# Kernel tuning notes

Measured on AMD Instinct MI355X. Metric: run time of the kernel, lower is better.

## Reference

```python
import jax, jax.numpy as jnp
import numpy as np

N_CLASS = 50257
EMB = 512
HID = 512
B = 64
T = 256


def setup_inputs() -> dict:
    key = jax.random.key(0)
    ks = jax.random.split(key, 12)
    K = 1.0 / np.sqrt(HID)
    u = lambda k, shape: jax.random.uniform(k, shape, jnp.float32) * K
    return {
        "X": jax.random.randint(ks[0], (B, T), 0, N_CLASS, jnp.int32),
        "emb": jax.random.normal(ks[1], (N_CLASS, EMB), jnp.float32),
        "w_ih0": u(ks[2], (4 * HID, EMB)),
        "w_hh0": u(ks[3], (4 * HID, HID)),
        "b_ih0": u(ks[4], (4 * HID,)),
        "b_hh0": u(ks[5], (4 * HID,)),
        "w_ih1": u(ks[6], (4 * HID, HID)),
        "w_hh1": u(ks[7], (4 * HID, HID)),
        "b_ih1": u(ks[8], (4 * HID,)),
        "b_hh1": u(ks[9], (4 * HID,)),
        "W": jax.random.normal(ks[10], (N_CLASS, HID), jnp.float32) / np.sqrt(HID),
        "b": jnp.ones((N_CLASS,), jnp.float32),
    }


def _lstm_layer(x, w_ih, w_hh, b_ih, b_hh):
    # x: [B, T, in] -> outputs: [B, T, H]; gate order i, f, g, o (as in source slicing)
    H = w_hh.shape[1]
    # precompute input contribution + both biases for all timesteps (one big GEMM)
    xg = jnp.einsum("bti,gi->btg", x, w_ih) + b_ih + b_hh  # [B, T, 4H]

    def step(carry, xg_t):
        h, c = carry
        g = xg_t + h @ w_hh.T  # [B, 4H]
        i_t = jax.nn.sigmoid(g[:, :H])
        f_t = jax.nn.sigmoid(g[:, H:2 * H])
        g_t = jnp.tanh(g[:, 2 * H:3 * H])
        o_t = jax.nn.sigmoid(g[:, 3 * H:])
        c = f_t * c + i_t * g_t
        h = o_t * jnp.tanh(c)
        return (h, c), h

    bsz = x.shape[0]
    init = (jnp.zeros((bsz, H), x.dtype), jnp.zeros((bsz, H), x.dtype))
    _, ys = jax.lax.scan(step, init, jnp.swapaxes(xg, 0, 1))  # [T, B, H]
    return jnp.swapaxes(ys, 0, 1)


def reference(X, emb, w_ih0, w_hh0, b_ih0, b_hh0, w_ih1, w_hh1, b_ih1, b_hh1, W, b):
    x = emb[X]  # [B, T, EMB] embedding lookup
    h0 = _lstm_layer(x, w_ih0, w_hh0, b_ih0, b_hh0)   # layer 0
    h1 = _lstm_layer(h0, w_ih1, w_hh1, b_ih1, b_hh1)  # layer 1 (input = layer0 output)
    last = h1[:, -1, :]  # last timestep, [B, H]
    return last @ W.T + b  # [B, N_CLASS]
```

## Files before the change

kernel.cpp:

```cpp
#include <hip/hip_runtime.h>
#include <cstdint>
#include <cstddef>

#define HH 512
#define BB 64
#define TT 256
#define GG 2048
#define NCLS 50257
#define NWG 128

typedef __attribute__((ext_vector_type(4))) float f32x4;
typedef __attribute__((ext_vector_type(8))) short bf16x8;
typedef __attribute__((ext_vector_type(4))) unsigned int u32x4;
typedef __attribute__((ext_vector_type(8))) unsigned int u32x8;

__device__ __forceinline__ unsigned short bf16_rn(float x){
    unsigned u = __float_as_uint(x);
    unsigned r = u + 0x7fffu + ((u >> 16) & 1u);
    return (unsigned short)(r >> 16);
}
__device__ __forceinline__ void split2(float x, unsigned short& hi, unsigned short& lo){
    unsigned short h = bf16_rn(x);
    float hf = __uint_as_float(((unsigned)h) << 16);
    lo = bf16_rn(x - hf);
    hi = h;
}
__device__ __forceinline__ bf16x8 mk8(unsigned a, unsigned b, unsigned c, unsigned d){
    u32x4 t; t[0]=a; t[1]=b; t[2]=c; t[3]=d;
    return __builtin_bit_cast(bf16x8, t);
}

__global__ __launch_bounds__(256) void split_bf16_k(
    const float* __restrict__ in, unsigned short* __restrict__ hi,
    unsigned short* __restrict__ lo, int n)
{
    int i = blockIdx.x * 256 + threadIdx.x;
    if (i < n){ unsigned short h, l; split2(in[i], h, l); hi[i] = h; lo[i] = l; }
}

__global__ __launch_bounds__(256,1) void lstm_scan_mfma(
    const float* __restrict__ xg,
    const unsigned short* __restrict__ Whi,
    const unsigned short* __restrict__ Wlo,
    unsigned* __restrict__ hpk,
    float* __restrict__ hseq,
    int* __restrict__ bar,
    int mode)
{
    __shared__ float gs[BB][17];
    const int tid  = threadIdx.x;
    const int lane = tid & 63, wv = tid >> 6;
    const int wg   = blockIdx.x;
    const int j0   = wg * 4;
    const int c16  = lane & 15, kg = lane >> 4;

    bf16x8 wbh[16], wbl[16];
    {
        const int grow = (c16 >> 2) * HH + j0 + (c16 & 3);
        const unsigned short* ph = Whi + (size_t)grow * HH + kg * 8;
        const unsigned short* pl = Wlo + (size_t)grow * HH + kg * 8;
        #pragma unroll
        for (int kt = 0; kt < 16; kt++){
            wbh[kt] = *(const bf16x8*)(ph + kt * 32);
            wbl[kt] = *(const bf16x8*)(pl + kt * 32);
        }
    }

    const int arow = wv * 16 + c16;
    const int xcol = (c16 >> 2) * HH + j0 + (c16 & 3);
    const int b0   = wv * 16 + kg * 4;
    const int ab   = tid >> 2, ad = tid & 3;

    float c_st = 0.f;

    f32x4 cur;
    {
        const float* xp = xg + xcol;
        cur[0] = xp[(size_t)(b0 + 0) * GG];
        cur[1] = xp[(size_t)(b0 + 1) * GG];
        cur[2] = xp[(size_t)(b0 + 2) * GG];
        cur[3] = xp[(size_t)(b0 + 3) * GG];
    }

    for (int t = 0; t < TT; t++){
        const unsigned* hin  = hpk + (size_t)(t & 1) * BB * HH;
        unsigned*       hout = hpk + (size_t)((t + 1) & 1) * BB * HH;

        f32x4 acc = cur;
        const unsigned* pa = hin + (size_t)arow * HH + kg * 8;
        #pragma unroll
        for (int kt = 0; kt < 16; kt++){
            u32x8 w = *(const u32x8*)(pa + kt * 32);
            unsigned h01 = __builtin_amdgcn_perm(w[1], w[0], 0x05040100u);
            unsigned h23 = __builtin_amdgcn_perm(w[3], w[2], 0x05040100u);
            unsigned h45 = __builtin_amdgcn_perm(w[5], w[4], 0x05040100u);
            unsigned h67 = __builtin_amdgcn_perm(w[7], w[6], 0x05040100u);
            unsigned l01 = __builtin_amdgcn_perm(w[1], w[0], 0x07060302u);
            unsigned l23 = __builtin_amdgcn_perm(w[3], w[2], 0x07060302u);
            unsigned l45 = __builtin_amdgcn_perm(w[5], w[4], 0x07060302u);
            unsigned l67 = __builtin_amdgcn_perm(w[7], w[6], 0x07060302u);
            bf16x8 a_h = mk8(h01, h23, h45, h67);
            bf16x8 a_l = mk8(l01, l23, l45, l67);
            acc = __builtin_amdgcn_mfma_f32_16x16x32_bf16(a_h, wbh[kt], acc, 0, 0, 0);
            acc = __builtin_amdgcn_mfma_f32_16x16x32_bf16(a_h, wbl[kt], acc, 0, 0, 0);
            acc = __builtin_amdgcn_mfma_f32_16x16x32_bf16(a_l, wbh[kt], acc, 0, 0, 0);
        }
        gs[b0 + 0][c16] = acc[0];
        gs[b0 + 1][c16] = acc[1];
        gs[b0 + 2][c16] = acc[2];
        gs[b0 + 3][c16] = acc[3];
        __syncthreads();
        {
            float gi = gs[ab][ad], gf = gs[ab][4 + ad], gg = gs[ab][8 + ad], go = gs[ab][12 + ad];
            gi = 1.f / (1.f + expf(-gi));
            gf = 1.f / (1.f + expf(-gf));
            gg = tanhf(gg);
            go = 1.f / (1.f + expf(-go));
            c_st = gf * c_st + gi * gg;
            float h = go * tanhf(c_st);
            unsigned short hb, lb; split2(h, hb, lb);
            unsigned pk = (((unsigned)lb) << 16) | (unsigned)hb;
            __hip_atomic_store(&hout[(size_t)ab * HH + j0 + ad], pk,
                               __ATOMIC_RELAXED, __HIP_MEMORY_SCOPE_AGENT);
            if (mode) hseq[(size_t)ab * TT * HH + (size_t)t * HH + j0 + ad] = h;
            else      hseq[(size_t)ab * HH + j0 + ad] = h;
        }
        __syncthreads();
        if (tid == 0){
            const int g = wg & 7;
            int old = __hip_atomic_fetch_add(bar + 32 + g * 32, 1,
                        __ATOMIC_RELAXED, __HIP_MEMORY_SCOPE_AGENT);
            if (old == (NWG / 8) * (t + 1) - 1){
                int r = __hip_atomic_fetch_add(bar + 288, 1,
                            __ATOMIC_RELAXED, __HIP_MEMORY_SCOPE_AGENT);
                if (r == 8 * (t + 1) - 1){
                    __hip_atomic_store(bar, t + 1,
                        __ATOMIC_RELAXED, __HIP_MEMORY_SCOPE_AGENT);
                }
            }
        }
        {
            const int tp = (t + 1 < TT) ? t + 1 : t;
            const float* xp = xg + (size_t)tp * BB * GG + xcol;
            cur[0] = xp[(size_t)(b0 + 0) * GG];
            cur[1] = xp[(size_t)(b0 + 1) * GG];
            cur[2] = xp[(size_t)(b0 + 2) * GG];
            cur[3] = xp[(size_t)(b0 + 3) * GG];
        }
        if (tid == 0){
            while (__hip_atomic_load(bar, __ATOMIC_RELAXED, __HIP_MEMORY_SCOPE_AGENT) < t + 1)
                __builtin_amdgcn_s_sleep(2);
            __builtin_amdgcn_fence(__ATOMIC_ACQUIRE, "agent");
        }
        __syncthreads();
    }
}

__global__ __launch_bounds__(256,2) void gemm_xg(
    const float* __restrict__ A, const int* __restrict__ gather,
    const float* __restrict__ Bw, const float* __restrict__ bias1,
    const float* __restrict__ bias2, float* __restrict__ out, int K)
{
    __shared__ float As[32][132];
    __shared__ float Bs[32][132];
    const int tid = threadIdx.x;
    const int row0 = blockIdx.y * 128, col0 = blockIdx.x * 128;
    const int tx = tid & 15, ty = tid >> 4;
    float acc[8][8];
    #pragma unroll
    for (int i=0;i<8;i++)
        #pragma unroll
        for (int j=0;j<8;j++) acc[i][j]=0.f;

    for (int k0=0;k0<K;k0+=32){
        #pragma unroll
        for (int i=0;i<4;i++){
            int f = tid + i*256;
            int r = f>>3, kq = f&7;
            const int grow = row0 + r;
            const float* src = gather ? (A + (size_t)gather[grow]*K)
                                      : (A + (size_t)grow*K);
            float4 v = *(const float4*)(src + k0 + kq*4);
            As[kq*4+0][r]=v.x; As[kq*4+1][r]=v.y; As[kq*4+2][r]=v.z; As[kq*4+3][r]=v.w;
        }
        #pragma unroll
        for (int i=0;i<4;i++){
            int f = tid + i*256;
            int r = f>>3, kq = f&7;
            const float* src = Bw + (size_t)(col0 + r)*K;
            float4 v = *(const float4*)(src + k0 + kq*4);
            Bs[kq*4+0][r]=v.x; Bs[kq*4+1][r]=v.y; Bs[kq*4+2][r]=v.z; Bs[kq*4+3][r]=v.w;
        }
        __syncthreads();
        #pragma unroll
        for (int kk=0;kk<32;kk++){
            float4 a03 = *(float4*)&As[kk][ty*8];
            float4 a47 = *(float4*)&As[kk][ty*8+4];
            float4 b03 = *(float4*)&Bs[kk][tx*8];
            float4 b47 = *(float4*)&Bs[kk][tx*8+4];
            float a[8] = {a03.x,a03.y,a03.z,a03.w,a47.x,a47.y,a47.z,a47.w};
            float b[8] = {b03.x,b03.y,b03.z,b03.w,b47.x,b47.y,b47.z,b47.w};
            #pragma unroll
            for (int i=0;i<8;i++)
                #pragma unroll
                for (int j=0;j<8;j++) acc[i][j] += a[i]*b[j];
        }
        __syncthreads();
    }
    #pragma unroll
    for (int i=0;i<8;i++){
        int r = row0 + ty*8 + i;
        int b = r >> 8, t = r & 255;
        float* orow = out + (size_t)(t*BB + b)*GG + col0 + tx*8;
        #pragma unroll
        for (int j=0;j<8;j++){
            int col = col0 + tx*8 + j;
            orow[j] = acc[i][j] + bias1[col] + bias2[col];
        }
    }
}

__global__ __launch_bounds__(256) void gemm_logits(
    const float* __restrict__ hlast, const float* __restrict__ W,
    const float* __restrict__ bias, float* __restrict__ out)
{
    __shared__ float As[32][68];
    __shared__ float Bs[32][68];
    const int tid = threadIdx.x;
    const int col0 = blockIdx.x * 64;
    const int tx = tid & 15, ty = tid >> 4;
    float acc[4][4];
    #pragma unroll
    for (int i=0;i<4;i++)
        #pragma unroll
        for (int j=0;j<4;j++) acc[i][j]=0.f;

    for (int k0=0;k0<HH;k0+=32){
        #pragma unroll
        for (int i=0;i<2;i++){
            int f = tid + i*256;
            int r = f>>3, kq = f&7;
            float4 v = *(const float4*)(hlast + (size_t)r*HH + k0 + kq*4);
            As[kq*4+0][r]=v.x; As[kq*4+1][r]=v.y; As[kq*4+2][r]=v.z; As[kq*4+3][r]=v.w;
        }
        #pragma unroll
        for (int i=0;i<2;i++){
            int f = tid + i*256;
            int r = f>>3, kq = f&7;
            int vrow = col0 + r;
            float4 v = make_float4(0.f,0.f,0.f,0.f);
            if (vrow < NCLS) v = *(const float4*)(W + (size_t)vrow*HH + k0 + kq*4);
            Bs[kq*4+0][r]=v.x; Bs[kq*4+1][r]=v.y; Bs[kq*4+2][r]=v.z; Bs[kq*4+3][r]=v.w;
        }
        __syncthreads();
        #pragma unroll
        for (int kk=0;kk<32;kk++){
            float4 a4 = *(float4*)&As[kk][ty*4];
            float4 b4 = *(float4*)&Bs[kk][tx*4];
            float a[4] = {a4.x,a4.y,a4.z,a4.w};
            float b[4] = {b4.x,b4.y,b4.z,b4.w};
            #pragma unroll
            for (int i=0;i<4;i++)
                #pragma unroll
                for (int j=0;j<4;j++) acc[i][j] += a[i]*b[j];
        }
        __syncthreads();
    }
    #pragma unroll
    for (int i=0;i<4;i++){
        int b = ty*4 + i;
        #pragma unroll
        for (int j=0;j<4;j++){
            int v = col0 + tx*4 + j;
            if (v < NCLS) out[(size_t)b*NCLS + v] = acc[i][j] + bias[v];
        }
    }
}

extern "C" void kernel_launch(void* const* d_in, const int* in_sizes, int n_in,
                              void* d_out, int out_size, void* d_ws, size_t ws_size,
                              hipStream_t stream)
{
    const int*   X     = (const int*)  d_in[0];
    const float* emb   = (const float*)d_in[1];
    const float* w_ih0 = (const float*)d_in[2];
    const float* w_hh0 = (const float*)d_in[3];
    const float* b_ih0 = (const float*)d_in[4];
    const float* b_hh0 = (const float*)d_in[5];
    const float* w_ih1 = (const float*)d_in[6];
    const float* w_hh1 = (const float*)d_in[7];
    const float* b_ih1 = (const float*)d_in[8];
    const float* b_hh1 = (const float*)d_in[9];
    const float* Wout  = (const float*)d_in[10];
    const float* bout  = (const float*)d_in[11];
    float* out = (float*)d_out;

    float* ws    = (float*)d_ws;
    float* xg    = ws;
    float* h0seq = ws + 33554432;
    float* hlast = ws + 41943040;
    unsigned short* Whi0 = (unsigned short*)(ws + 41975808);
    unsigned short* Wlo0 = (unsigned short*)(ws + 42500096);
    unsigned short* Whi1 = (unsigned short*)(ws + 43024384);
    unsigned short* Wlo1 = (unsigned short*)(ws + 43548672);
    unsigned*       hpk  = (unsigned*)(ws + 44072960);
    int*            bar  = (int*)(ws + 44138496);

    dim3 gemmGrid(16, 128);

    split_bf16_k<<<4096, 256, 0, stream>>>(w_hh0, Whi0, Wlo0, GG*HH);
    split_bf16_k<<<4096, 256, 0, stream>>>(w_hh1, Whi1, Wlo1, GG*HH);

    gemm_xg<<<gemmGrid, 256, 0, stream>>>(emb, X, w_ih0, b_ih0, b_hh0, xg, HH);
    hipMemsetAsync(hpk, 0, (size_t)2*BB*HH*sizeof(unsigned), stream);
    hipMemsetAsync(bar, 0, 4096, stream);
    {
        const float* a0 = xg; const unsigned short *a1 = Whi0, *a2 = Wlo0;
        unsigned* a3 = hpk; float* a4 = h0seq; int* a5 = bar; int a6 = 1;
        void* args[] = {&a0,&a1,&a2,&a3,&a4,&a5,&a6};
        hipLaunchCooperativeKernel((void*)lstm_scan_mfma, dim3(NWG), dim3(256), args, 0, stream);
    }
    gemm_xg<<<gemmGrid, 256, 0, stream>>>(h0seq, nullptr, w_ih1, b_ih1, b_hh1, xg, HH);
    hipMemsetAsync(hpk, 0, (size_t)2*BB*HH*sizeof(unsigned), stream);
    hipMemsetAsync(bar, 0, 4096, stream);
    {
        const float* a0 = xg; const unsigned short *a1 = Whi1, *a2 = Wlo1;
        unsigned* a3 = hpk; float* a4 = hlast; int* a5 = bar; int a6 = 0;
        void* args[] = {&a0,&a1,&a2,&a3,&a4,&a5,&a6};
        hipLaunchCooperativeKernel((void*)lstm_scan_mfma, dim3(NWG), dim3(256), args, 0, stream);
    }
    gemm_logits<<<786, 256, 0, stream>>>(hlast, Wout, bout, out);
}
```

Measured before the change: 4.944 ms.

## Use split-bf16 MFMA for input-projection GEMMs and stage recurrent weights in LDS

Replaces the scalar fp32 tiled input-projection GEMM with an MFMA kernel that uses a three-product hi/lo bf16 split, which keeps roughly fp32 accuracy. Layer-0 output is now stored as packed hi/lo bf16 so the layer-1 GEMM reads it without converting. The recurrent kernel moves its weight fragments from registers into LDS and splits accumulation across two accumulators so consecutive MFMAs do not depend on each other. Workspace buffers for the split weights are reused sequentially, which adds extra split launches and LDS reads on every timestep.

```diff
diff --git a/kernel.cpp b/kernel.cpp
--- a/kernel.cpp
+++ b/kernel.cpp
@@ -9,6 +9,9 @@
 #define NCLS 50257
 #define NWG 128
 
+#define PERM_HI 0x05040100u
+#define PERM_LO 0x07060302u
+
 typedef __attribute__((ext_vector_type(4))) float f32x4;
 typedef __attribute__((ext_vector_type(8))) short bf16x8;
 typedef __attribute__((ext_vector_type(4))) unsigned int u32x4;
@@ -38,15 +41,132 @@
     if (i < n){ unsigned short h, l; split2(in[i], h, l); hi[i] = h; lo[i] = l; }
 }
 
+__global__ __launch_bounds__(256,2) void gemm_xg_mfma(
+    const float* __restrict__ Af32, const unsigned* __restrict__ Apk,
+    const int* __restrict__ gather,
+    const unsigned short* __restrict__ Bhi, const unsigned short* __restrict__ Blo,
+    const float* __restrict__ bias1, const float* __restrict__ bias2,
+    float* __restrict__ out)
+{
+    __shared__ unsigned short Ah[128][40], Al[128][40], Bh[128][40], Bl[128][40];
+    const int tid  = threadIdx.x;
+    const int lane = tid & 63, wid = tid >> 6;
+    const int c16  = lane & 15, kg = lane >> 4;
+    const int row0 = blockIdx.y * 128, col0 = blockIdx.x * 128;
+    const int wm = (wid >> 1) * 64, wn = (wid & 1) * 64;
+    const int sr = tid & 127;
+    const bool isA = tid < 128;
+
+    f32x4 acc[4][4];
+    #pragma unroll
+    for (int mi=0;mi<4;mi++)
+        #pragma unroll
+        for (int ni=0;ni<4;ni++){ acc[mi][ni][0]=0.f; acc[mi][ni][1]=0.f; acc[mi][ni][2]=0.f; acc[mi][ni][3]=0.f; }
+
+    for (int ks = 0; ks < 16; ks++){
+        const int k0 = ks * 32;
+        if (isA){
+            if (Apk){
+                const unsigned* src = Apk + (size_t)(row0 + sr) * HH + k0;
+                u32x4 v[8];
+                #pragma unroll
+                for (int q=0;q<8;q++) v[q] = *(const u32x4*)(src + q*4);
+                #pragma unroll
+                for (int g=0; g<4; g++){
+                    u32x4 h4, l4;
+                    h4[0]=__builtin_amdgcn_perm(v[2*g][1],   v[2*g][0],   PERM_HI);
+                    h4[1]=__builtin_amdgcn_perm(v[2*g][3],   v[2*g][2],   PERM_HI);
+                    h4[2]=__builtin_amdgcn_perm(v[2*g+1][1], v[2*g+1][0], PERM_HI);
+                    h4[3]=__builtin_amdgcn_perm(v[2*g+1][3], v[2*g+1][2], PERM_HI);
+                    l4[0]=__builtin_amdgcn_perm(v[2*g][1],   v[2*g][0],   PERM_LO);
+                    l4[1]=__builtin_amdgcn_perm(v[2*g][3],   v[2*g][2],   PERM_LO);
+                    l4[2]=__builtin_amdgcn_perm(v[2*g+1][1], v[2*g+1][0], PERM_LO);
+                    l4[3]=__builtin_amdgcn_perm(v[2*g+1][3], v[2*g+1][2], PERM_LO);
+                    *(u32x4*)&Ah[sr][g*8] = h4;
+                    *(u32x4*)&Al[sr][g*8] = l4;
+                }
+            } else {
+                const float* src = Af32 + (size_t)gather[row0 + sr] * HH + k0;
+                float f[32];
+                #pragma unroll
+                for (int q=0;q<8;q++) *(float4*)&f[q*4] = *(const float4*)(src + q*4);
+                #pragma unroll
+                for (int g=0; g<4; g++){
+                    unsigned short h[8], l[8];
+                    #pragma unroll
+                    for (int j=0;j<8;j++) split2(f[g*8+j], h[j], l[j]);
+                    u32x4 h4, l4;
+                    #pragma unroll
+                    for (int q=0;q<4;q++){
+                        h4[q] = (((unsigned)h[2*q+1])<<16) | (unsigned)h[2*q];
+                        l4[q] = (((unsigned)l[2*q+1])<<16) | (unsigned)l[2*q];
+                    }
+                    *(u32x4*)&Ah[sr][g*8] = h4;
+                    *(u32x4*)&Al[sr][g*8] = l4;
+                }
+            }
+        } else {
+            const unsigned short* sh = Bhi + (size_t)(col0 + sr) * HH + k0;
+            const unsigned short* sl = Blo + (size_t)(col0 + sr) * HH + k0;
+            #pragma unroll
+            for (int g=0; g<4; g++){
+                *(u32x4*)&Bh[sr][g*8] = *(const u32x4*)(sh + g*8);
+                *(u32x4*)&Bl[sr][g*8] = *(const u32x4*)(sl + g*8);
+            }
+        }
+        __syncthreads();
+
+        bf16x8 ah[4], al[4];
+        #pragma unroll
+        for (int mi=0;mi<4;mi++){
+            ah[mi] = *(const bf16x8*)&Ah[wm + mi*16 + c16][kg*8];
+            al[mi] = *(const bf16x8*)&Al[wm + mi*16 + c16][kg*8];
+        }
+        #pragma unroll
+        for (int ni=0;ni<4;ni++){
+            bf16x8 bh = *(const bf16x8*)&Bh[wn + ni*16 + c16][kg*8];
+            bf16x8 bl = *(const bf16x8*)&Bl[wn + ni*16 + c16][kg*8];
+            #pragma unroll
+            for (int mi=0;mi<4;mi++){
+                acc[mi][ni] = __builtin_amdgcn_mfma_f32_16x16x32_bf16(ah[mi], bh, acc[mi][ni], 0,0,0);
+                acc[mi][ni] = __builtin_amdgcn_mfma_f32_16x16x32_bf16(ah[mi], bl, acc[mi][ni], 0,0,0);
+                acc[mi][ni] = __builtin_amdgcn_mfma_f32_16x16x32_bf16(al[mi], bh, acc[mi][ni], 0,0,0);
+            }
+        }
+        __syncthreads();
+    }
+    float bs[4];
+    #pragma unroll
+    for (int ni=0;ni<4;ni++){
+        int c = col0 + wn + ni*16 + c16;
+        bs[ni] = bias1[c] + bias2[c];
+    }
+    #pragma unroll
+    for (int mi=0;mi<4;mi++){
+        #pragma unroll
+        for (int i=0;i<4;i++){
+            int R = row0 + wm + mi*16 + kg*4 + i;
+            int b = R >> 8, t = R & 255;
+            float* op = out + (size_t)(t*BB + b)*GG + col0 + wn;
+            #pragma unroll
+            for (int ni=0;ni<4;ni++)
+                op[ni*16 + c16] = acc[mi][ni][i] + bs[ni];
+        }
+    }
+}
+
 __global__ __launch_bounds__(256,1) void lstm_scan_mfma(
     const float* __restrict__ xg,
     const unsigned short* __restrict__ Whi,
     const unsigned short* __restrict__ Wlo,
     unsigned* __restrict__ hpk,
-    float* __restrict__ hseq,
+    unsigned* __restrict__ hseq_pk,
+    float* __restrict__ hlast,
     int* __restrict__ bar,
     int mode)
 {
+    __shared__ unsigned short Wh[8192];
+    __shared__ unsigned short Wl[8192];
     __shared__ float gs[BB][17];
     const int tid  = threadIdx.x;
     const int lane = tid & 63, wv = tid >> 6;
@@ -54,17 +174,18 @@
     const int j0   = wg * 4;
     const int c16  = lane & 15, kg = lane >> 4;
 
-    bf16x8 wbh[16], wbl[16];
     {
-        const int grow = (c16 >> 2) * HH + j0 + (c16 & 3);
-        const unsigned short* ph = Whi + (size_t)grow * HH + kg * 8;
-        const unsigned short* pl = Wlo + (size_t)grow * HH + kg * 8;
-        #pragma unroll
-        for (int kt = 0; kt < 16; kt++){
-            wbh[kt] = *(const bf16x8*)(ph + kt * 32);
-            wbl[kt] = *(const bf16x8*)(pl + kt * 32);
-        }
-    }
+        const int rr = tid >> 4, kseg = tid & 15;
+        const int grow = (rr >> 2) * HH + j0 + (rr & 3);
+        const unsigned short* ph = Whi + (size_t)grow * HH + kseg * 32;
+        const unsigned short* pl = Wlo + (size_t)grow * HH + kseg * 32;
+        #pragma unroll
+        for (int g=0; g<4; g++){
+            *(u32x4*)&Wh[((kseg*4 + g)*16 + rr)*8] = *(const u32x4*)(ph + g*8);
+            *(u32x4*)&Wl[((kseg*4 + g)*16 + rr)*8] = *(const u32x4*)(pl + g*8);
+        }
+    }
+    __syncthreads();
 
     const int arow = wv * 16 + c16;
     const int xcol = (c16 >> 2) * HH + j0 + (c16 & 3);
@@ -86,29 +207,38 @@
         const unsigned* hin  = hpk + (size_t)(t & 1) * BB * HH;
         unsigned*       hout = hpk + (size_t)((t + 1) & 1) * BB * HH;
 
-        f32x4 acc = cur;
+        f32x4 acc0 = cur;
+        f32x4 acc1; acc1[0]=0.f; acc1[1]=0.f; acc1[2]=0.f; acc1[3]=0.f;
         const unsigned* pa = hin + (size_t)arow * HH + kg * 8;
         #pragma unroll
         for (int kt = 0; kt < 16; kt++){
             u32x8 w = *(const u32x8*)(pa + kt * 32);
-            unsigned h01 = __builtin_amdgcn_perm(w[1], w[0], 0x05040100u);
-            unsigned h23 = __builtin_amdgcn_perm(w[3], w[2], 0x05040100u);
-            unsigned h45 = __builtin_amdgcn_perm(w[5], w[4], 0x05040100u);
-            unsigned h67 = __builtin_amdgcn_perm(w[7], w[6], 0x05040100u);
-            unsigned l01 = __builtin_amdgcn_perm(w[1], w[0], 0x07060302u);
-            unsigned l23 = __builtin_amdgcn_perm(w[3], w[2], 0x07060302u);
-            unsigned l45 = __builtin_amdgcn_perm(w[5], w[4], 0x07060302u);
-            unsigned l67 = __builtin_amdgcn_perm(w[7], w[6], 0x07060302u);
+            unsigned h01 = __builtin_amdgcn_perm(w[1], w[0], PERM_HI);
+            unsigned h23 = __builtin_amdgcn_perm(w[3], w[2], PERM_HI);
+            unsigned h45 = __builtin_amdgcn_perm(w[5], w[4], PERM_HI);
+            unsigned h67 = __builtin_amdgcn_perm(w[7], w[6], PERM_HI);
+            unsigned l01 = __builtin_amdgcn_perm(w[1], w[0], PERM_LO);
+            unsigned l23 = __builtin_amdgcn_perm(w[3], w[2], PERM_LO);
+            unsigned l45 = __builtin_amdgcn_perm(w[5], w[4], PERM_LO);
+            unsigned l67 = __builtin_amdgcn_perm(w[7], w[6], PERM_LO);
             bf16x8 a_h = mk8(h01, h23, h45, h67);
             bf16x8 a_l = mk8(l01, l23, l45, l67);
-            acc = __builtin_amdgcn_mfma_f32_16x16x32_bf16(a_h, wbh[kt], acc, 0, 0, 0);
-            acc = __builtin_amdgcn_mfma_f32_16x16x32_bf16(a_h, wbl[kt], acc, 0, 0, 0);
-            acc = __builtin_amdgcn_mfma_f32_16x16x32_bf16(a_l, wbh[kt], acc, 0, 0, 0);
-        }
-        gs[b0 + 0][c16] = acc[0];
-        gs[b0 + 1][c16] = acc[1];
-        gs[b0 + 2][c16] = acc[2];
-        gs[b0 + 3][c16] = acc[3];
+            bf16x8 wbh = *(const bf16x8*)&Wh[((kt*4 + kg)*16 + c16)*8];
+            bf16x8 wbl = *(const bf16x8*)&Wl[((kt*4 + kg)*16 + c16)*8];
+            if (kt & 1){
+                acc1 = __builtin_amdgcn_mfma_f32_16x16x32_bf16(a_h, wbh, acc1, 0,0,0);
+                acc1 = __builtin_amdgcn_mfma_f32_16x16x32_bf16(a_h, wbl, acc1, 0,0,0);
+                acc1 = __builtin_amdgcn_mfma_f32_16x16x32_bf16(a_l, wbh, acc1, 0,0,0);
+            } else {
+                acc0 = __builtin_amdgcn_mfma_f32_16x16x32_bf16(a_h, wbh, acc0, 0,0,0);
+                acc0 = __builtin_amdgcn_mfma_f32_16x16x32_bf16(a_h, wbl, acc0, 0,0,0);
+                acc0 = __builtin_amdgcn_mfma_f32_16x16x32_bf16(a_l, wbh, acc0, 0,0,0);
+            }
+        }
+        gs[b0 + 0][c16] = acc0[0] + acc1[0];
+        gs[b0 + 1][c16] = acc0[1] + acc1[1];
+        gs[b0 + 2][c16] = acc0[2] + acc1[2];
+        gs[b0 + 3][c16] = acc0[3] + acc1[3];
         __syncthreads();
         {
             float gi = gs[ab][ad], gf = gs[ab][4 + ad], gg = gs[ab][8 + ad], go = gs[ab][12 + ad];
@@ -122,8 +252,8 @@
             unsigned pk = (((unsigned)lb) << 16) | (unsigned)hb;
             __hip_atomic_store(&hout[(size_t)ab * HH + j0 + ad], pk,
                                __ATOMIC_RELAXED, __HIP_MEMORY_SCOPE_AGENT);
-            if (mode) hseq[(size_t)ab * TT * HH + (size_t)t * HH + j0 + ad] = h;
-            else      hseq[(size_t)ab * HH + j0 + ad] = h;
+            if (mode) hseq_pk[(size_t)(ab * TT + t) * HH + j0 + ad] = pk;
+            else      hlast[(size_t)ab * HH + j0 + ad] = h;
         }
         __syncthreads();
         if (tid == 0){
@@ -153,70 +283,6 @@
             __builtin_amdgcn_fence(__ATOMIC_ACQUIRE, "agent");
         }
         __syncthreads();
-    }
-}
-
-__global__ __launch_bounds__(256,2) void gemm_xg(
-    const float* __restrict__ A, const int* __restrict__ gather,
-    const float* __restrict__ Bw, const float* __restrict__ bias1,
-    const float* __restrict__ bias2, float* __restrict__ out, int K)
-{
-    __shared__ float As[32][132];
-    __shared__ float Bs[32][132];
-    const int tid = threadIdx.x;
-    const int row0 = blockIdx.y * 128, col0 = blockIdx.x * 128;
-    const int tx = tid & 15, ty = tid >> 4;
-    float acc[8][8];
-    #pragma unroll
-    for (int i=0;i<8;i++)
-        #pragma unroll
-        for (int j=0;j<8;j++) acc[i][j]=0.f;
-
-    for (int k0=0;k0<K;k0+=32){
-        #pragma unroll
-        for (int i=0;i<4;i++){
-            int f = tid + i*256;
-            int r = f>>3, kq = f&7;
-            const int grow = row0 + r;
-            const float* src = gather ? (A + (size_t)gather[grow]*K)
-                                      : (A + (size_t)grow*K);
-            float4 v = *(const float4*)(src + k0 + kq*4);
-            As[kq*4+0][r]=v.x; As[kq*4+1][r]=v.y; As[kq*4+2][r]=v.z; As[kq*4+3][r]=v.w;
-        }
-        #pragma unroll
-        for (int i=0;i<4;i++){
-            int f = tid + i*256;
-            int r = f>>3, kq = f&7;
-            const float* src = Bw + (size_t)(col0 + r)*K;
-            float4 v = *(const float4*)(src + k0 + kq*4);
-            Bs[kq*4+0][r]=v.x; Bs[kq*4+1][r]=v.y; Bs[kq*4+2][r]=v.z; Bs[kq*4+3][r]=v.w;
-        }
-        __syncthreads();
-        #pragma unroll
-        for (int kk=0;kk<32;kk++){
-            float4 a03 = *(float4*)&As[kk][ty*8];
-            float4 a47 = *(float4*)&As[kk][ty*8+4];
-            float4 b03 = *(float4*)&Bs[kk][tx*8];
-            float4 b47 = *(float4*)&Bs[kk][tx*8+4];
-            float a[8] = {a03.x,a03.y,a03.z,a03.w,a47.x,a47.y,a47.z,a47.w};
-            float b[8] = {b03.x,b03.y,b03.z,b03.w,b47.x,b47.y,b47.z,b47.w};
-            #pragma unroll
-            for (int i=0;i<8;i++)
-                #pragma unroll
-                for (int j=0;j<8;j++) acc[i][j] += a[i]*b[j];
-        }
-        __syncthreads();
-    }
-    #pragma unroll
-    for (int i=0;i<8;i++){
-        int r = row0 + ty*8 + i;
-        int b = r >> 8, t = r & 255;
-        float* orow = out + (size_t)(t*BB + b)*GG + col0 + tx*8;
-        #pragma unroll
-        for (int j=0;j<8;j++){
-            int col = col0 + tx*8 + j;
-            orow[j] = acc[i][j] + bias1[col] + bias2[col];
-        }
     }
 }
 
@@ -295,38 +361,37 @@
     const float* bout  = (const float*)d_in[11];
     float* out = (float*)d_out;
 
-    float* ws    = (float*)d_ws;
-    float* xg    = ws;
-    float* h0seq = ws + 33554432;
-    float* hlast = ws + 41943040;
-    unsigned short* Whi0 = (unsigned short*)(ws + 41975808);
-    unsigned short* Wlo0 = (unsigned short*)(ws + 42500096);
-    unsigned short* Whi1 = (unsigned short*)(ws + 43024384);
-    unsigned short* Wlo1 = (unsigned short*)(ws + 43548672);
-    unsigned*       hpk  = (unsigned*)(ws + 44072960);
-    int*            bar  = (int*)(ws + 44138496);
+    float* ws = (float*)d_ws;
+    float*          xg      = ws;
+    unsigned*       hseq_pk = (unsigned*)(ws + 33554432);
+    float*          hlast   = ws + 41943040;
+    unsigned short* Shi     = (unsigned short*)(ws + 41975808);
+    unsigned short* Slo     = (unsigned short*)(ws + 42500096);
+    unsigned*       hpk     = (unsigned*)(ws + 43024384);
+    int*            bar     = (int*)(ws + 43089920);
 
     dim3 gemmGrid(16, 128);
 
-    split_bf16_k<<<4096, 256, 0, stream>>>(w_hh0, Whi0, Wlo0, GG*HH);
-    split_bf16_k<<<4096, 256, 0, stream>>>(w_hh1, Whi1, Wlo1, GG*HH);
-
-    gemm_xg<<<gemmGrid, 256, 0, stream>>>(emb, X, w_ih0, b_ih0, b_hh0, xg, HH);
+    split_bf16_k<<<4096, 256, 0, stream>>>(w_ih0, Shi, Slo, GG*HH);
+    gemm_xg_mfma<<<gemmGrid, 256, 0, stream>>>(emb, nullptr, X, Shi, Slo, b_ih0, b_hh0, xg);
+    split_bf16_k<<<4096, 256, 0, stream>>>(w_hh0, Shi, Slo, GG*HH);
     hipMemsetAsync(hpk, 0, (size_t)2*BB*HH*sizeof(unsigned), stream);
     hipMemsetAsync(bar, 0, 4096, stream);
     {
-        const float* a0 = xg; const unsigned short *a1 = Whi0, *a2 = Wlo0;
-        unsigned* a3 = hpk; float* a4 = h0seq; int* a5 = bar; int a6 = 1;
-        void* args[] = {&a0,&a1,&a2,&a3,&a4,&a5,&a6};
+        const float* a0 = xg; const unsigned short *a1 = Shi, *a2 = Slo;
+        unsigned* a3 = hpk; unsigned* a4 = hseq_pk; float* a5 = hlast; int* a6 = bar; int a7 = 1;
+        void* args[] = {&a0,&a1,&a2,&a3,&a4,&a5,&a6,&a7};
         hipLaunchCooperativeKernel((void*)lstm_scan_mfma, dim3(NWG), dim3(256), args, 0, stream);
     }
-    gemm_xg<<<gemmGrid, 256, 0, stream>>>(h0seq, nullptr, w_ih1, b_ih1, b_hh1, xg, HH);
+    split_bf16_k<<<4096, 256, 0, stream>>>(w_ih1, Shi, Slo, GG*HH);
+    gemm_xg_mfma<<<gemmGrid, 256, 0, stream>>>(nullptr, hseq_pk, nullptr, Shi, Slo, b_ih1, b_hh1, xg);
+    split_bf16_k<<<4096, 256, 0, stream>>>(w_hh1, Shi, Slo, GG*HH);
     hipMemsetAsync(hpk, 0, (size_t)2*BB*HH*sizeof(unsigned), stream);
     hipMemsetAsync(bar, 0, 4096, stream);
     {
-        const float* a0 = xg; const unsigned short *a1 = Whi1, *a2 = Wlo1;
-        unsigned* a3 = hpk; float* a4 = hlast; int* a5 = bar; int a6 = 0;
-        void* args[] = {&a0,&a1,&a2,&a3,&a4,&a5,&a6};
+        const float* a0 = xg; const unsigned short *a1 = Shi, *a2 = Slo;
+        unsigned* a3 = hpk; unsigned* a4 = hseq_pk; float* a5 = hlast; int* a6 = bar; int a7 = 0;
+        void* args[] = {&a0,&a1,&a2,&a3,&a4,&a5,&a6,&a7};
         hipLaunchCooperativeKernel((void*)lstm_scan_mfma, dim3(NWG), dim3(256), args, 0, stream);
     }
     gemm_logits<<<786, 256, 0, stream>>>(hlast, Wout, bout, out);
```

After: 5.550 ms. +12.3%, slower.
